# Optimization experiments

Hardware: AMD Instinct MI355X
Metric: run time of the kernel (lower is better)

Reference implementation:

```python
import jax, jax.numpy as jnp
import numpy as np

B, N, D, H = 2, 2048, 1024, 16
HD = D // H
SCALE = HD ** -0.5


def setup_inputs() -> dict:
    key = jax.random.key(0)
    ks = jax.random.split(key, 5)
    s = D ** -0.5  # keep activations well-scaled like torch Linear init
    return {
        "x": jax.random.normal(ks[0], (B, N, D), jnp.float32),
        "Wq": jax.random.normal(ks[1], (D, D), jnp.float32) * s,
        "bq": jnp.zeros((D,), jnp.float32),
        "Wk": jax.random.normal(ks[2], (D, D), jnp.float32) * s,
        "bk": jnp.zeros((D,), jnp.float32),
        "Wv": jax.random.normal(ks[3], (D, D), jnp.float32) * s,
        "bv": jnp.zeros((D,), jnp.float32),
        "Wo": jax.random.normal(ks[4], (D, D), jnp.float32) * s,
        "bo": jnp.zeros((D,), jnp.float32),
    }


def reference(x, Wq, bq, Wk, bk, Wv, bv, Wo, bo):
    # projections: [B,N,D] -> [B,H,N,HD]
    def split_heads(t):
        return t.reshape(B, N, H, HD).transpose(0, 2, 1, 3)

    q = split_heads(x @ Wq + bq)
    k = split_heads(x @ Wk + bk)
    v = split_heads(x @ Wv + bv)
    # eager attention: explicit [B,H,N,N] scores, matching the torch module
    attn = jnp.einsum("bhnd,bhmd->bhnm", q, k) * SCALE
    attn = jax.nn.softmax(attn, axis=-1)
    out = jnp.einsum("bhnm,bhmd->bhnd", attn, v)
    out = out.transpose(0, 2, 1, 3).reshape(B, N, D)
    return out @ Wo + bo
```

## Files before the change

### kernel.cpp

```cpp
#include <hip/hip_runtime.h>
#include <hip/hip_bf16.h>

typedef __attribute__((ext_vector_type(8))) short bf16x8;
typedef __attribute__((ext_vector_type(4))) float f32x4;
typedef __attribute__((ext_vector_type(4))) unsigned short us4;
typedef __attribute__((ext_vector_type(8))) unsigned short us8;
typedef unsigned short u16;

#define NB 2
#define NSEQ 2048
#define DM 1024
#define NH 16
#define HD 64
#define NTOK (NB*NSEQ)
#define QK_SCALE (0.125f * 1.4426950408889634f)

__device__ __forceinline__ u16 f2b(float f) {
  __hip_bfloat16 h = __float2bfloat16(f);
  return __builtin_bit_cast(u16, h);
}

__device__ __forceinline__ unsigned pkbf(float a, float b) {
  return (unsigned)f2b(a) | ((unsigned)f2b(b) << 16);
}

__device__ __forceinline__ void gload16(const void* g, void* l) {
  __builtin_amdgcn_global_load_lds((__attribute__((address_space(1))) void*)g,
                                   (__attribute__((address_space(3))) void*)l, 16, 0, 0);
}

__global__ __launch_bounds__(256) void k_convx(const float* __restrict__ x, u16* __restrict__ xb) {
  const int idx = (blockIdx.x * 256 + threadIdx.x) * 8;
  const float4 v0 = *(const float4*)(x + idx);
  const float4 v1 = *(const float4*)(x + idx + 4);
  us8 o;
  o[0]=f2b(v0.x); o[1]=f2b(v0.y); o[2]=f2b(v0.z); o[3]=f2b(v0.w);
  o[4]=f2b(v1.x); o[5]=f2b(v1.y); o[6]=f2b(v1.z); o[7]=f2b(v1.w);
  *(us8*)(xb + idx) = o;
}

__global__ __launch_bounds__(256) void k_twt4(const float* __restrict__ W0, const float* __restrict__ W1,
                                              const float* __restrict__ W2, const float* __restrict__ W3,
                                              u16* __restrict__ T0, u16* __restrict__ T1,
                                              u16* __restrict__ T2, u16* __restrict__ T3) {
  const float* W = (blockIdx.z == 0) ? W0 : (blockIdx.z == 1) ? W1 : (blockIdx.z == 2) ? W2 : W3;
  u16* WT = (blockIdx.z == 0) ? T0 : (blockIdx.z == 1) ? T1 : (blockIdx.z == 2) ? T2 : T3;
  __shared__ float tile[64][68];
  const int n0 = blockIdx.x * 64, k0 = blockIdx.y * 64;
  const int tr = threadIdx.x >> 4, tc = (threadIdx.x & 15) * 4;
#pragma unroll
  for (int rr = 0; rr < 4; ++rr) {
    const int r = rr * 16 + tr;
    *(float4*)&tile[r][tc] = *(const float4*)&W[(size_t)(k0 + r) * DM + n0 + tc];
  }
  __syncthreads();
#pragma unroll
  for (int rr = 0; rr < 4; ++rr) {
    const int nr = rr * 16 + tr;
    us4 o;
#pragma unroll
    for (int e = 0; e < 4; ++e) o[e] = f2b(tile[tc + e][nr]);
    *(us4*)&WT[(size_t)(n0 + nr) * DM + k0 + tc] = o;
  }
}

template<int MODE>
__global__ __launch_bounds__(256) void k_gemm(
    const u16* __restrict__ A, const u16* __restrict__ A1,
    const u16* __restrict__ Bt,
    const float* __restrict__ bias, const float* __restrict__ bias1,
    void* __restrict__ out0, void* __restrict__ out1,
    float scale0, float scale1)
{
  const u16* Ap = A; const float* bp = bias; void* outp = out0; float scale = scale0;
  if (MODE == 0 && blockIdx.z == 1) { Ap = A1; bp = bias1; outp = out1; scale = scale1; }

  __shared__ char smem[64 * 1024];
  const int tid = threadIdx.x, lane = tid & 63, wv = tid >> 6;
  const int li = lane & 15, g = lane >> 4;
  const int wi = wv >> 1, wj = wv & 1;
  const int i0 = blockIdx.y * 128, j0 = blockIdx.x * 128;

  f32x4 acc[4][4];
#pragma unroll
  for (int a = 0; a < 4; ++a)
#pragma unroll
    for (int b = 0; b < 4; ++b) acc[a][b] = f32x4{0.f, 0.f, 0.f, 0.f};

  auto stage = [&](int kt, int buf) {
#pragma unroll
    for (int c = 0; c < 4; ++c) {
      const int lg = c * 256 + tid;
      const int r = lg >> 3, ch = (lg & 7) ^ (r & 7);
      gload16(Ap + (size_t)(i0 + r) * 1024 + kt * 64 + ch * 8,
              smem + buf * 32768 + (c * 256 + wv * 64) * 16);
      gload16(Bt + (size_t)(j0 + r) * 1024 + kt * 64 + ch * 8,
              smem + buf * 32768 + 16384 + (c * 256 + wv * 64) * 16);
    }
  };

  stage(0, 0);

  for (int kt = 0; kt < 16; ++kt) {
    __syncthreads();
    if (kt + 1 < 16) stage(kt + 1, (kt + 1) & 1);
    const char* As = smem + (kt & 1) * 32768;
    const char* Bs = As + 16384;
#pragma unroll
    for (int ks = 0; ks < 2; ++ks) {
      bf16x8 af[4], bfr[4];
#pragma unroll
      for (int it = 0; it < 4; ++it) {
        const int ri = 64 * wi + 16 * it + li;
        af[it] = *(const bf16x8*)(As + ri * 128 + ((ks * 64 + g * 16) ^ ((ri & 7) << 4)));
        const int rj = 64 * wj + 16 * it + li;
        bfr[it] = *(const bf16x8*)(Bs + rj * 128 + ((ks * 64 + g * 16) ^ ((rj & 7) << 4)));
      }
#pragma unroll
      for (int it = 0; it < 4; ++it)
#pragma unroll
        for (int jt = 0; jt < 4; ++jt)
          acc[it][jt] = __builtin_amdgcn_mfma_f32_16x16x32_bf16(af[it], bfr[jt], acc[it][jt], 0, 0, 0);
    }
  }

#pragma unroll
  for (int it = 0; it < 4; ++it) {
    const int ib = i0 + 64 * wi + 16 * it + 4 * g;
    f32x4 b4;
    if constexpr (MODE != 1) b4 = *(const f32x4*)(bp + ib);
#pragma unroll
    for (int jt = 0; jt < 4; ++jt) {
      const int j = j0 + 64 * wj + 16 * jt + li;
      f32x4 v = acc[it][jt];
      if constexpr (MODE == 1) {
        const float bj = bp[j];
        v[0] += bj; v[1] += bj; v[2] += bj; v[3] += bj;
      } else {
        v += b4;
      }
      if constexpr (MODE == 0) {
        v *= scale;
        us4 pk; pk[0]=f2b(v[0]); pk[1]=f2b(v[1]); pk[2]=f2b(v[2]); pk[3]=f2b(v[3]);
        *(us4*)((u16*)outp + (size_t)j * 1024 + ib) = pk;
      } else if constexpr (MODE == 1) {
        us4 pk; pk[0]=f2b(v[0]); pk[1]=f2b(v[1]); pk[2]=f2b(v[2]); pk[3]=f2b(v[3]);
        const size_t addr = ((size_t)(ib >> 11) * 1024 + j) * 2048 + (ib & 2047);
        *(us4*)((u16*)outp + addr) = pk;
      } else {
        *(f32x4*)((float*)outp + (size_t)j * 1024 + ib) = v;
      }
    }
  }
}

__global__ __launch_bounds__(256, 2) void k_attn(const u16* __restrict__ Q, const u16* __restrict__ K,
                                                 const u16* __restrict__ Vt, u16* __restrict__ O)
{
  __shared__ char smem[48 * 1024];
  const int tid = threadIdx.x, lane = tid & 63, w = tid >> 6;
  const int li = lane & 15, g = lane >> 4;
  const int bh = blockIdx.y, b = bh >> 4, h = bh & 15;
  const int n0 = blockIdx.x * 128;
  const size_t tokbase = (size_t)b * NSEQ;
  const int iq = 16 * w + li;

  bf16x8 qf[2][2];
#pragma unroll
  for (int grp = 0; grp < 2; ++grp)
#pragma unroll
    for (int ks = 0; ks < 2; ++ks)
      qf[grp][ks] = *(const bf16x8*)(Q + (tokbase + n0 + 64 * grp + iq) * 1024 + h * 64 + 32 * ks + 8 * g);

  bf16x8 ones;
#pragma unroll
  for (int e = 0; e < 8; ++e) ones[e] = (short)0x3F80;

  f32x4 oacc[2][4];
#pragma unroll
  for (int grp = 0; grp < 2; ++grp)
#pragma unroll
    for (int dt = 0; dt < 4; ++dt) oacc[grp][dt] = f32x4{0.f, 0.f, 0.f, 0.f};
  f32x4 ls[2] = {f32x4{0.f,0.f,0.f,0.f}, f32x4{0.f,0.f,0.f,0.f}};

  const u16* Kb = K + tokbase * 1024 + h * 64;
  const u16* Vb = Vt + (size_t)bh * 64 * 2048;

  auto stage = [&](int t, int buf) {
    const int jn = t * 64;
#pragma unroll
    for (int c = 0; c < 2; ++c) {
      const int lg = c * 256 + tid;
      const int r = lg >> 3, ch = (lg & 7) ^ (r & 7);
      gload16(Kb + (size_t)(jn + r) * 1024 + ch * 8, smem + buf * 8192 + (c * 256 + w * 64) * 16);
      gload16(Vb + (size_t)r * 2048 + jn + ch * 8, smem + 16384 + buf * 8192 + (c * 256 + w * 64) * 16);
    }
  };

  auto tilebody = [&](int t, int buf) {
    __syncthreads();
    if (t + 1 < 32) stage(t + 1, buf ^ 1);
    const char* Ks = smem + buf * 8192;
    const char* Vs = smem + 16384 + buf * 8192;

    f32x4 s[2][4];
#pragma unroll
    for (int grp = 0; grp < 2; ++grp)
#pragma unroll
      for (int jt = 0; jt < 4; ++jt) s[grp][jt] = f32x4{0.f, 0.f, 0.f, 0.f};
#pragma unroll
    for (int ks = 0; ks < 2; ++ks) {
#pragma unroll
      for (int jt = 0; jt < 4; ++jt) {
        const int rj = 16 * jt + li;
        bf16x8 a = *(const bf16x8*)(Ks + rj * 128 + ((ks * 64 + g * 16) ^ ((rj & 7) << 4)));
        s[0][jt] = __builtin_amdgcn_mfma_f32_16x16x32_bf16(a, qf[0][ks], s[0][jt], 0, 0, 0);
        s[1][jt] = __builtin_amdgcn_mfma_f32_16x16x32_bf16(a, qf[1][ks], s[1][jt], 0, 0, 0);
      }
    }

#pragma unroll
    for (int grp = 0; grp < 2; ++grp) {
      const int row = iq + 64 * grp;
      char* Pr = smem + 32768 + row * 128;
      const int swz = (row & 7) << 4;
#pragma unroll
      for (int jt = 0; jt < 4; ++jt) {
        uint2 pk;
        pk.x = pkbf(exp2f(s[grp][jt][0]), exp2f(s[grp][jt][1]));
        pk.y = pkbf(exp2f(s[grp][jt][2]), exp2f(s[grp][jt][3]));
        *(uint2*)(Pr + ((32 * jt + 8 * g) ^ swz)) = pk;
      }
    }

#pragma unroll
    for (int ks = 0; ks < 2; ++ks) {
      const int kb = ks * 64 + g * 16;
      bf16x8 bpv0 = *(const bf16x8*)(smem + 32768 + iq * 128 + (kb ^ ((iq & 7) << 4)));
      bf16x8 bpv1 = *(const bf16x8*)(smem + 32768 + (iq + 64) * 128 + (kb ^ ((iq & 7) << 4)));
      ls[0] = __builtin_amdgcn_mfma_f32_16x16x32_bf16(ones, bpv0, ls[0], 0, 0, 0);
      ls[1] = __builtin_amdgcn_mfma_f32_16x16x32_bf16(ones, bpv1, ls[1], 0, 0, 0);
#pragma unroll
      for (int dt = 0; dt < 4; ++dt) {
        const int rd = 16 * dt + li;
        bf16x8 av = *(const bf16x8*)(Vs + rd * 128 + (kb ^ ((rd & 7) << 4)));
        oacc[0][dt] = __builtin_amdgcn_mfma_f32_16x16x32_bf16(av, bpv0, oacc[0][dt], 0, 0, 0);
        oacc[1][dt] = __builtin_amdgcn_mfma_f32_16x16x32_bf16(av, bpv1, oacc[1][dt], 0, 0, 0);
      }
    }
  };

  stage(0, 0);
#pragma unroll 1
  for (int tt = 0; tt < 16; ++tt) {
    tilebody(2 * tt, 0);
    tilebody(2 * tt + 1, 1);
  }

#pragma unroll
  for (int grp = 0; grp < 2; ++grp) {
    const float inv = 1.f / ls[grp][0];
    const size_t obase = (tokbase + n0 + 64 * grp + iq) * 1024 + h * 64;
#pragma unroll
    for (int dt = 0; dt < 4; ++dt) {
      us4 pk;
#pragma unroll
      for (int e = 0; e < 4; ++e) pk[e] = f2b(oacc[grp][dt][e] * inv);
      *(us4*)(O + obase + 16 * dt + 4 * g) = pk;
    }
  }
}

extern "C" void kernel_launch(void* const* d_in, const int* in_sizes, int n_in,
                              void* d_out, int out_size, void* d_ws, size_t ws_size,
                              hipStream_t stream) {
  const float* x  = (const float*)d_in[0];
  const float* Wq = (const float*)d_in[1];
  const float* bq = (const float*)d_in[2];
  const float* Wk = (const float*)d_in[3];
  const float* bk = (const float*)d_in[4];
  const float* Wv = (const float*)d_in[5];
  const float* bv = (const float*)d_in[6];
  const float* Wo = (const float*)d_in[7];
  const float* bo = (const float*)d_in[8];

  char* ws = (char*)d_ws;
  u16* xb  = (u16*)(ws);
  u16* WqT = (u16*)(ws + (8  << 20));
  u16* WkT = (u16*)(ws + (10 << 20));
  u16* WvT = (u16*)(ws + (12 << 20));
  u16* WoT = (u16*)(ws + (14 << 20));
  u16* Qb  = (u16*)(ws + (16 << 20));
  u16* Kb  = (u16*)(ws + (24 << 20));
  u16* Vtb = (u16*)(ws + (32 << 20));
  u16* Ob  = (u16*)(ws + (40 << 20));

  k_convx<<<2048, 256, 0, stream>>>(x, xb);
  k_twt4<<<dim3(16, 16, 4), 256, 0, stream>>>(Wq, Wk, Wv, Wo, WqT, WkT, WvT, WoT);

  k_gemm<0><<<dim3(32, 8, 2), 256, 0, stream>>>(WqT, WkT, xb, bq, bk, Qb, Kb, QK_SCALE, 1.0f);
  k_gemm<1><<<dim3(8, 32, 1), 256, 0, stream>>>(xb, nullptr, WvT, bv, nullptr, Vtb, nullptr, 1.0f, 1.0f);

  k_attn<<<dim3(16, 32), 256, 0, stream>>>(Qb, Kb, Vtb, Ob);

  k_gemm<2><<<dim3(32, 8, 1), 256, 0, stream>>>(WoT, nullptr, Ob, bo, nullptr, d_out, nullptr, 1.0f, 1.0f);
}
```

Baseline: 131.1 us.

## Keep softmax probabilities in registers via 16x16x16 MFMA and shrink attention blocks

The attention kernel drops the LDS round-trip for the P matrix. The exp2 results stay in registers and feed 16x16x16 bf16 MFMAs directly, since the QK accumulator layout matches the B operand of the k=16 instruction. Blocks shrink to 2 waves covering 64 queries, the grid doubles to 1024 blocks, and block IDs are remapped so blocks sharing a batch-head are grouped together, probably for cache locality. The cost is twice as many MFMA instructions at half K depth, and each K/V tile is now reused by fewer queries per block.

```diff
diff --git a/kernel.cpp b/kernel.cpp
--- a/kernel.cpp
+++ b/kernel.cpp
@@ -2,6 +2,7 @@
 #include <hip/hip_bf16.h>
 
 typedef __attribute__((ext_vector_type(8))) short bf16x8;
+typedef __attribute__((ext_vector_type(4))) short bf16x4;
 typedef __attribute__((ext_vector_type(4))) float f32x4;
 typedef __attribute__((ext_vector_type(4))) unsigned short us4;
 typedef __attribute__((ext_vector_type(8))) unsigned short us8;
@@ -20,9 +21,14 @@
   return __builtin_bit_cast(u16, h);
 }
 
-__device__ __forceinline__ unsigned pkbf(float a, float b) {
-  return (unsigned)f2b(a) | ((unsigned)f2b(b) << 16);
-}
+#if __has_builtin(__builtin_amdgcn_mfma_f32_16x16x16bf16_1k)
+#define MFMA16(c, a, b) c = __builtin_amdgcn_mfma_f32_16x16x16bf16_1k(a, b, c, 0, 0, 0)
+#elif __has_builtin(__builtin_amdgcn_mfma_f32_16x16x16_bf16)
+typedef __attribute__((ext_vector_type(4))) __bf16 bf16v4;
+#define MFMA16(c, a, b) c = __builtin_amdgcn_mfma_f32_16x16x16_bf16(__builtin_bit_cast(bf16v4, a), __builtin_bit_cast(bf16v4, b), c, 0, 0, 0)
+#else
+#define MFMA16(c, a, b) asm volatile("s_nop 1\n\tv_mfma_f32_16x16x16_bf16 %0, %1, %2, %0\n\ts_nop 7\n\ts_nop 7" : "+v"(c) : "v"(a), "v"(b))
+#endif
 
 __device__ __forceinline__ void gload16(const void* g, void* l) {
   __builtin_amdgcn_global_load_lds((__attribute__((address_space(1))) void*)g,
@@ -154,27 +160,30 @@
   }
 }
 
-__global__ __launch_bounds__(256, 2) void k_attn(const u16* __restrict__ Q, const u16* __restrict__ K,
+__global__ __launch_bounds__(128, 2) void k_attn(const u16* __restrict__ Q, const u16* __restrict__ K,
                                                  const u16* __restrict__ Vt, u16* __restrict__ O)
 {
-  __shared__ char smem[48 * 1024];
+  __shared__ char smem[32 * 1024];
   const int tid = threadIdx.x, lane = tid & 63, w = tid >> 6;
   const int li = lane & 15, g = lane >> 4;
-  const int bh = blockIdx.y, b = bh >> 4, h = bh & 15;
-  const int n0 = blockIdx.x * 128;
+
+  const int vid = blockIdx.x + 32 * blockIdx.y;
+  const int bh = (vid & 7) * 4 + (vid >> 8);
+  const int qt = (vid >> 3) & 31;
+  const int b = bh >> 4, h = bh & 15;
+  const int n0 = qt * 64;
   const size_t tokbase = (size_t)b * NSEQ;
-  const int iq = 16 * w + li;
 
   bf16x8 qf[2][2];
 #pragma unroll
   for (int grp = 0; grp < 2; ++grp)
 #pragma unroll
     for (int ks = 0; ks < 2; ++ks)
-      qf[grp][ks] = *(const bf16x8*)(Q + (tokbase + n0 + 64 * grp + iq) * 1024 + h * 64 + 32 * ks + 8 * g);
-
-  bf16x8 ones;
-#pragma unroll
-  for (int e = 0; e < 8; ++e) ones[e] = (short)0x3F80;
+      qf[grp][ks] = *(const bf16x8*)(Q + (tokbase + n0 + 32 * w + 16 * grp + li) * 1024 + h * 64 + 32 * ks + 8 * g);
+
+  bf16x4 ones4;
+#pragma unroll
+  for (int e = 0; e < 4; ++e) ones4[e] = (short)0x3F80;
 
   f32x4 oacc[2][4];
 #pragma unroll
@@ -189,11 +198,11 @@
   auto stage = [&](int t, int buf) {
     const int jn = t * 64;
 #pragma unroll
-    for (int c = 0; c < 2; ++c) {
-      const int lg = c * 256 + tid;
+    for (int c = 0; c < 4; ++c) {
+      const int lg = c * 128 + tid;
       const int r = lg >> 3, ch = (lg & 7) ^ (r & 7);
-      gload16(Kb + (size_t)(jn + r) * 1024 + ch * 8, smem + buf * 8192 + (c * 256 + w * 64) * 16);
-      gload16(Vb + (size_t)r * 2048 + jn + ch * 8, smem + 16384 + buf * 8192 + (c * 256 + w * 64) * 16);
+      gload16(Kb + (size_t)(jn + r) * 1024 + ch * 8, smem + buf * 8192 + (c * 128 + w * 64) * 16);
+      gload16(Vb + (size_t)r * 2048 + jn + ch * 8, smem + 16384 + buf * 8192 + (c * 128 + w * 64) * 16);
     }
   };
 
@@ -219,33 +228,28 @@
       }
     }
 
-#pragma unroll
-    for (int grp = 0; grp < 2; ++grp) {
-      const int row = iq + 64 * grp;
-      char* Pr = smem + 32768 + row * 128;
-      const int swz = (row & 7) << 4;
+    bf16x4 bpv[2][4];
+#pragma unroll
+    for (int grp = 0; grp < 2; ++grp)
 #pragma unroll
       for (int jt = 0; jt < 4; ++jt) {
-        uint2 pk;
-        pk.x = pkbf(exp2f(s[grp][jt][0]), exp2f(s[grp][jt][1]));
-        pk.y = pkbf(exp2f(s[grp][jt][2]), exp2f(s[grp][jt][3]));
-        *(uint2*)(Pr + ((32 * jt + 8 * g) ^ swz)) = pk;
-      }
-    }
-
-#pragma unroll
-    for (int ks = 0; ks < 2; ++ks) {
-      const int kb = ks * 64 + g * 16;
-      bf16x8 bpv0 = *(const bf16x8*)(smem + 32768 + iq * 128 + (kb ^ ((iq & 7) << 4)));
-      bf16x8 bpv1 = *(const bf16x8*)(smem + 32768 + (iq + 64) * 128 + (kb ^ ((iq & 7) << 4)));
-      ls[0] = __builtin_amdgcn_mfma_f32_16x16x32_bf16(ones, bpv0, ls[0], 0, 0, 0);
-      ls[1] = __builtin_amdgcn_mfma_f32_16x16x32_bf16(ones, bpv1, ls[1], 0, 0, 0);
-#pragma unroll
-      for (int dt = 0; dt < 4; ++dt) {
-        const int rd = 16 * dt + li;
-        bf16x8 av = *(const bf16x8*)(Vs + rd * 128 + (kb ^ ((rd & 7) << 4)));
-        oacc[0][dt] = __builtin_amdgcn_mfma_f32_16x16x32_bf16(av, bpv0, oacc[0][dt], 0, 0, 0);
-        oacc[1][dt] = __builtin_amdgcn_mfma_f32_16x16x32_bf16(av, bpv1, oacc[1][dt], 0, 0, 0);
+        bf16x4 pv;
+#pragma unroll
+        for (int e = 0; e < 4; ++e) pv[e] = (short)f2b(exp2f(s[grp][jt][e]));
+        bpv[grp][jt] = pv;
+        MFMA16(ls[grp], ones4, pv);
+      }
+
+#pragma unroll
+    for (int dt = 0; dt < 4; ++dt) {
+      const int rd = 16 * dt + li;
+      const char* Vr = Vs + rd * 128;
+      const int swz = (rd & 7) << 4;
+#pragma unroll
+      for (int jt = 0; jt < 4; ++jt) {
+        bf16x4 av = *(const bf16x4*)(Vr + ((32 * jt + 8 * g) ^ swz));
+        MFMA16(oacc[0][dt], av, bpv[0][jt]);
+        MFMA16(oacc[1][dt], av, bpv[1][jt]);
       }
     }
   };
@@ -260,7 +264,7 @@
 #pragma unroll
   for (int grp = 0; grp < 2; ++grp) {
     const float inv = 1.f / ls[grp][0];
-    const size_t obase = (tokbase + n0 + 64 * grp + iq) * 1024 + h * 64;
+    const size_t obase = (tokbase + n0 + 32 * w + 16 * grp + li) * 1024 + h * 64;
 #pragma unroll
     for (int dt = 0; dt < 4; ++dt) {
       us4 pk;
@@ -301,7 +305,7 @@
   k_gemm<0><<<dim3(32, 8, 2), 256, 0, stream>>>(WqT, WkT, xb, bq, bk, Qb, Kb, QK_SCALE, 1.0f);
   k_gemm<1><<<dim3(8, 32, 1), 256, 0, stream>>>(xb, nullptr, WvT, bv, nullptr, Vtb, nullptr, 1.0f, 1.0f);
 
-  k_attn<<<dim3(16, 32), 256, 0, stream>>>(Qb, Kb, Vtb, Ob);
+  k_attn<<<dim3(32, 32), 128, 0, stream>>>(Qb, Kb, Vtb, Ob);
 
   k_gemm<2><<<dim3(32, 8, 1), 256, 0, stream>>>(WoT, nullptr, Ob, bo, nullptr, d_out, nullptr, 1.0f, 1.0f);
 }
```

New measurement: 136.3 us. 1.04x slower.
